# Kernel tuning notes

Hardware: AMD Instinct MI355X
Metric: run time of the kernel (lower is better)

## Reference

```python
import jax, jax.numpy as jnp
import numpy as np

N_HEAD = 16
HEAD_DIM = 64  # n_embd // n_head = 1024 // 16


def setup_inputs() -> dict:
    key = jax.random.key(0)
    k1, k2, k3 = jax.random.split(key, 3)
    B, T, C = 4, 2048, 1024
    x = jax.random.normal(k1, (B, T, C), dtype=jnp.float32)
    # torch Linear weight is (out, in); we store transposed (in, out) for x @ W
    w_qkv = jax.random.normal(k2, (C, 3 * C), dtype=jnp.float32) * (1.0 / np.sqrt(C))
    w_out = jax.random.normal(k3, (C, C), dtype=jnp.float32) * (1.0 / np.sqrt(C))
    return {"x": x, "w_qkv": w_qkv, "w_out": w_out}


def reference(x, w_qkv, w_out):
    B, T, C = x.shape
    scale = 1.0 / np.sqrt(HEAD_DIM).astype(np.float32)
    qkv = x @ w_qkv                                   # [B, T, 3C]
    q, k, v = jnp.split(qkv, 3, axis=2)
    def heads(t):  # [B, T, C] -> [B, H, T, Dh]
        return t.reshape(B, T, N_HEAD, HEAD_DIM).transpose(0, 2, 1, 3)
    q, k, v = heads(q), heads(k), heads(v)
    att = jnp.einsum('bhqd,bhkd->bhqk', q, k) * scale  # [B, H, T, T]
    causal = jnp.tril(jnp.ones((T, T), dtype=bool))
    att = jnp.where(causal[None, None], att, jnp.float32(-jnp.inf))
    att = jax.nn.softmax(att, axis=-1)
    y = jnp.einsum('bhqk,bhkd->bhqd', att, v)          # [B, H, T, Dh]
    y = y.transpose(0, 2, 1, 3).reshape(B, T, C)
    return y @ w_out
```

## Files before the change

### kernel.cpp

```cpp
#include <hip/hip_runtime.h>
#include <hip/hip_bf16.h>

#define B_ 4
#define T_ 2048
#define C_ 1024
#define H_ 16
#define D_ 64

typedef __bf16 bf16x8 __attribute__((ext_vector_type(8)));
typedef float f32x4 __attribute__((ext_vector_type(4)));

__device__ __forceinline__ unsigned short f2bs(float f) {
    __hip_bfloat16 h = __float2bfloat16(f);
    return *reinterpret_cast<unsigned short*>(&h);
}

__device__ __forceinline__ int swz(int row, int col) {
    return (row * 64 + col) ^ ((row & 7) << 3);
}

__device__ __forceinline__ void gload16(const void* g, void* l) {
    auto gp = (const __attribute__((address_space(1))) void*)(g);
    auto lp = (__attribute__((address_space(3))) void*)(uintptr_t)(l);
    __builtin_amdgcn_global_load_lds(gp, lp, 16, 0, 0);
}

__global__ __launch_bounds__(256)
void cvt_f32_to_bf16(const float* __restrict__ in, unsigned short* __restrict__ out, int n4) {
    int i = blockIdx.x * 256 + threadIdx.x;
    if (i >= n4) return;
    float4 v = ((const float4*)in)[i];
    union { unsigned short h[4]; uint2 u; } pk;
    pk.h[0] = f2bs(v.x); pk.h[1] = f2bs(v.y);
    pk.h[2] = f2bs(v.z); pk.h[3] = f2bs(v.w);
    ((uint2*)out)[i] = pk.u;
}

__global__ __launch_bounds__(256)
void transpose_to_bf16(const float* __restrict__ in, unsigned short* __restrict__ out,
                       int R, int C) {
    __shared__ float tile[64][65];
    const int tx = threadIdx.x & 63;
    const int ty = threadIdx.x >> 6;
    const int r0 = blockIdx.y * 64, c0 = blockIdx.x * 64;
    #pragma unroll
    for (int i = 0; i < 16; ++i) {
        int r = ty * 16 + i;
        tile[r][tx] = in[(size_t)(r0 + r) * C + c0 + tx];
    }
    __syncthreads();
    #pragma unroll
    for (int i = 0; i < 16; ++i) {
        int r = ty * 16 + i;
        out[(size_t)(c0 + r) * R + r0 + tx] = f2bs(tile[tx][r]);
    }
}

template<int MODE>
__global__ __launch_bounds__(256)
void gemm_bt(const unsigned short* __restrict__ A,
             const unsigned short* __restrict__ Bt,
             float* __restrict__ Out, int N_out,
             unsigned short* __restrict__ Qb,
             unsigned short* __restrict__ Kb,
             unsigned short* __restrict__ Vt,
             int K) {
    __shared__ alignas(16) unsigned short As[128 * 64];
    __shared__ alignas(16) unsigned short Bs[128 * 64];
    const int tid = threadIdx.x;
    const int l = tid & 63;
    const int c16 = l & 15, lq = l >> 4;
    const int wv = tid >> 6;
    const int wrow = wv >> 1, wcol = wv & 1;
    const int m0 = blockIdx.x * 128, n0 = blockIdx.y * 128;

    f32x4 acc[4][4];
    #pragma unroll
    for (int i = 0; i < 4; ++i)
        #pragma unroll
        for (int j = 0; j < 4; ++j)
            acc[i][j] = f32x4{0.f, 0.f, 0.f, 0.f};

    const int srow = tid >> 3;
    const int scs  = tid & 7;
    const int ldsbase = (tid & ~63) * 8;

    for (int k0 = 0; k0 < K; k0 += 64) {
        __syncthreads();
        #pragma unroll
        for (int p = 0; p < 4; ++p) {
            int row = p * 32 + srow;
            int csw = 8 * (scs ^ (row & 7));
            gload16(&A[(size_t)(m0 + row) * K + k0 + csw], &As[p * 2048 + ldsbase]);
            gload16(&Bt[(size_t)(n0 + row) * K + k0 + csw], &Bs[p * 2048 + ldsbase]);
        }
        __syncthreads();
        #pragma unroll
        for (int kk = 0; kk < 64; kk += 32) {
            bf16x8 af[4], bfv[4];
            int koff = kk + lq * 8;
            #pragma unroll
            for (int i = 0; i < 4; ++i) {
                af[i]  = *(const bf16x8*)&As[swz(wrow * 64 + i * 16 + c16, koff)];
                bfv[i] = *(const bf16x8*)&Bs[swz(wcol * 64 + i * 16 + c16, koff)];
            }
            #pragma unroll
            for (int mi = 0; mi < 4; ++mi)
                #pragma unroll
                for (int ni = 0; ni < 4; ++ni)
                    acc[mi][ni] = __builtin_amdgcn_mfma_f32_16x16x32_bf16(
                        af[mi], bfv[ni], acc[mi][ni], 0, 0, 0);
        }
    }

    #pragma unroll
    for (int mi = 0; mi < 4; ++mi) {
        #pragma unroll
        for (int ni = 0; ni < 4; ++ni) {
            #pragma unroll
            for (int r = 0; r < 4; ++r) {
                float v = acc[mi][ni][r];
                int row = m0 + wrow * 64 + mi * 16 + lq * 4 + r;
                int col = n0 + wcol * 64 + ni * 16 + c16;
                if (MODE == 1) {
                    Out[(size_t)row * N_out + col] = v;
                } else {
                    int which = col >> 10;
                    int c = col & 1023;
                    int h = c >> 6, d = c & 63;
                    int b = row >> 11, t = row & 2047;
                    int bh = b * H_ + h;
                    if (which == 0)
                        Qb[((size_t)(bh * T_ + t)) * D_ + d] = f2bs(v * 0.1803368801111204f);
                    else if (which == 1)
                        Kb[((size_t)(bh * T_ + t)) * D_ + d] = f2bs(v);
                    else
                        Vt[((size_t)(bh * D_ + d)) * T_ + t] = f2bs(v);
                }
            }
        }
    }
}

__global__ __launch_bounds__(256, 4)
void attn_fwd(const unsigned short* __restrict__ Qb,
              const unsigned short* __restrict__ Kb,
              const unsigned short* __restrict__ Vt,
              unsigned short* __restrict__ Y) {
    __shared__ alignas(16) unsigned short Ks[2][64 * 64];
    __shared__ alignas(16) unsigned short Vs[2][64 * 64];
    __shared__ alignas(16) unsigned short Pl[4][16 * 64];
    const int tid = threadIdx.x;
    const int wv = tid >> 6;
    const int l = tid & 63;
    const int c16 = l & 15, lq = l >> 4;
    const int bh = blockIdx.x & 63;
    const int qp = blockIdx.x >> 6;
    const unsigned short* Kp = Kb + (size_t)bh * T_ * D_;
    const unsigned short* Vp = Vt + (size_t)bh * D_ * T_;
    const unsigned short* Qbase = Qb + (size_t)bh * T_ * D_;
    const int b = bh >> 4, h = bh & 15;
    const int srow = tid >> 3;
    const int scs  = tid & 7;
    const int scol_sw = 8 * (scs ^ (srow & 7));
    const int wbase = wv * 512;
    unsigned short* Pw = (unsigned short*)Pl[wv];

    #pragma unroll
    for (int half = 0; half < 2; ++half) {
        const int qc = (half == 0) ? qp : 31 - qp;
        const int q0w = qc * 64 + wv * 16;
        const int nt = qc + 1;

        bf16x8 qf[2];
        #pragma unroll
        for (int ks = 0; ks < 2; ++ks)
            qf[ks] = *(const bf16x8*)&Qbase[(size_t)(q0w + c16) * 64 + 32 * ks + 8 * lq];

        f32x4 o[4];
        #pragma unroll
        for (int d0 = 0; d0 < 4; ++d0) o[d0] = f32x4{0.f, 0.f, 0.f, 0.f};
        float lsum = 0.f;

        __syncthreads();
        gload16(&Kp[(size_t)srow * 64 + scol_sw],        &Ks[0][wbase]);
        gload16(&Kp[(size_t)(srow + 32) * 64 + scol_sw], &Ks[0][2048 + wbase]);
        gload16(&Vp[(size_t)srow * T_ + scol_sw],        &Vs[0][wbase]);
        gload16(&Vp[(size_t)(srow + 32) * T_ + scol_sw], &Vs[0][2048 + wbase]);

        for (int it = 0; it < nt; ++it) {
            const int kb = it * 64;
            __syncthreads();
            if (it + 1 < nt) {
                const int kn = kb + 64;
                unsigned short* Kd = Ks[(it + 1) & 1];
                unsigned short* Vd = Vs[(it + 1) & 1];
                gload16(&Kp[(size_t)(kn + srow) * 64 + scol_sw],        &Kd[wbase]);
                gload16(&Kp[(size_t)(kn + srow + 32) * 64 + scol_sw],   &Kd[2048 + wbase]);
                gload16(&Vp[(size_t)srow * T_ + kn + scol_sw],          &Vd[wbase]);
                gload16(&Vp[(size_t)(srow + 32) * T_ + kn + scol_sw],   &Vd[2048 + wbase]);
            }
            const unsigned short* Kl = Ks[it & 1];
            const unsigned short* Vl = Vs[it & 1];

            f32x4 s[4];
            #pragma unroll
            for (int hh = 0; hh < 4; ++hh) s[hh] = f32x4{0.f, 0.f, 0.f, 0.f};
            __builtin_amdgcn_s_setprio(1);
            #pragma unroll
            for (int ks = 0; ks < 2; ++ks) {
                bf16x8 af[4];
                #pragma unroll
                for (int hh = 0; hh < 4; ++hh)
                    af[hh] = *(const bf16x8*)&Kl[swz(16 * hh + c16, 32 * ks + 8 * lq)];
                #pragma unroll
                for (int hh = 0; hh < 4; ++hh)
                    s[hh] = __builtin_amdgcn_mfma_f32_16x16x32_bf16(af[hh], qf[ks], s[hh], 0, 0, 0);
            }
            __builtin_amdgcn_s_setprio(0);
            if (it == nt - 1) {
                const int q = q0w + c16;
                #pragma unroll
                for (int hh = 0; hh < 4; ++hh)
                    #pragma unroll
                    for (int r = 0; r < 4; ++r)
                        if (kb + 16 * hh + 4 * lq + r > q) s[hh][r] = -1e30f;
            }
            float rs = 0.f;
            #pragma unroll
            for (int hh = 0; hh < 4; ++hh)
                #pragma unroll
                for (int r = 0; r < 4; ++r) {
                    float p = exp2f(s[hh][r]);
                    s[hh][r] = p;
                    rs += p;
                }
            lsum += rs;
            #pragma unroll
            for (int hh = 0; hh < 4; ++hh) {
                uint2 pk;
                pk.x = (unsigned)f2bs(s[hh][0]) | ((unsigned)f2bs(s[hh][1]) << 16);
                pk.y = (unsigned)f2bs(s[hh][2]) | ((unsigned)f2bs(s[hh][3]) << 16);
                *(uint2*)&Pw[swz(c16, 16 * hh + 4 * lq)] = pk;
            }
            __builtin_amdgcn_s_setprio(1);
            #pragma unroll
            for (int ks = 0; ks < 2; ++ks) {
                bf16x8 pb = *(const bf16x8*)&Pw[swz(c16, 32 * ks + 8 * lq)];
                #pragma unroll
                for (int d0 = 0; d0 < 4; ++d0) {
                    bf16x8 va = *(const bf16x8*)&Vl[swz(16 * d0 + c16, 32 * ks + 8 * lq)];
                    o[d0] = __builtin_amdgcn_mfma_f32_16x16x32_bf16(va, pb, o[d0], 0, 0, 0);
                }
            }
            __builtin_amdgcn_s_setprio(0);
        }

        float lt = lsum;
        lt += __shfl_xor(lt, 16);
        lt += __shfl_xor(lt, 32);
        float inv = 1.f / lt;
        int t = q0w + c16;
        #pragma unroll
        for (int d0 = 0; d0 < 4; ++d0) {
            uint2 w;
            w.x = (unsigned)f2bs(o[d0][0] * inv) | ((unsigned)f2bs(o[d0][1] * inv) << 16);
            w.y = (unsigned)f2bs(o[d0][2] * inv) | ((unsigned)f2bs(o[d0][3] * inv) << 16);
            *(uint2*)&Y[((size_t)(b * T_ + t)) * C_ + h * D_ + 16 * d0 + 4 * lq] = w;
        }
    }
}

extern "C" void kernel_launch(void* const* d_in, const int* in_sizes, int n_in,
                              void* d_out, int out_size, void* d_ws, size_t ws_size,
                              hipStream_t stream) {
    const float* x     = (const float*)d_in[0];
    const float* w_qkv = (const float*)d_in[1];
    const float* w_out = (const float*)d_in[2];
    float* out = (float*)d_out;
    char* ws = (char*)d_ws;

    unsigned short* xb  = (unsigned short*)(ws);
    unsigned short* wqt = (unsigned short*)(ws + (16u << 20));
    unsigned short* wot = (unsigned short*)(ws + (22u << 20));
    unsigned short* Qb  = (unsigned short*)(ws + (24u << 20));
    unsigned short* Kb  = (unsigned short*)(ws + (40u << 20));
    unsigned short* Vt  = (unsigned short*)(ws + (56u << 20));
    unsigned short* Yb  = (unsigned short*)(ws + (72u << 20));

    cvt_f32_to_bf16<<<8192, 256, 0, stream>>>(x, xb, (B_ * T_ * C_) / 4);
    transpose_to_bf16<<<dim3(48, 16), 256, 0, stream>>>(w_qkv, wqt, 1024, 3072);
    transpose_to_bf16<<<dim3(16, 16), 256, 0, stream>>>(w_out, wot, 1024, 1024);
    gemm_bt<0><<<dim3(64, 24), 256, 0, stream>>>(xb, wqt, nullptr, 3072, Qb, Kb, Vt, 1024);
    attn_fwd<<<1024, 256, 0, stream>>>(Qb, Kb, Vt, Yb);
    gemm_bt<1><<<dim3(64, 8), 256, 0, stream>>>(Yb, wot, out, 1024, nullptr, nullptr, nullptr, 1024);
}
```

Measured before the change: 186.5 us.

## Double-buffer GEMM LDS tiles and enlarge attention query tile to 128 rows

The GEMM now uses two LDS buffers so the next K-slice's global-to-LDS loads are issued before the current slice's MFMAs, which halves the barriers per iteration and overlaps load latency with compute. The attention kernel now has each wave handle 32 query rows (128 per block), reusing every loaded K/V tile for twice as many MFMAs. The grid is halved accordingly and waves skip fully masked key tiles. In exchange, register and LDS use per block grow, launch bounds drop to 2 blocks per SM, and fewer blocks may reduce latency hiding.

```diff
diff --git a/kernel.cpp b/kernel.cpp
--- a/kernel.cpp
+++ b/kernel.cpp
@@ -65,8 +65,8 @@
              unsigned short* __restrict__ Kb,
              unsigned short* __restrict__ Vt,
              int K) {
-    __shared__ alignas(16) unsigned short As[128 * 64];
-    __shared__ alignas(16) unsigned short Bs[128 * 64];
+    __shared__ alignas(16) unsigned short As[2][128 * 64];
+    __shared__ alignas(16) unsigned short Bs[2][128 * 64];
     const int tid = threadIdx.x;
     const int l = tid & 63;
     const int c16 = l & 15, lq = l >> 4;
@@ -85,24 +85,31 @@
     const int scs  = tid & 7;
     const int ldsbase = (tid & ~63) * 8;
 
-    for (int k0 = 0; k0 < K; k0 += 64) {
-        __syncthreads();
+    auto stage = [&](int k0, int buf) {
         #pragma unroll
         for (int p = 0; p < 4; ++p) {
             int row = p * 32 + srow;
             int csw = 8 * (scs ^ (row & 7));
-            gload16(&A[(size_t)(m0 + row) * K + k0 + csw], &As[p * 2048 + ldsbase]);
-            gload16(&Bt[(size_t)(n0 + row) * K + k0 + csw], &Bs[p * 2048 + ldsbase]);
-        }
+            gload16(&A[(size_t)(m0 + row) * K + k0 + csw], &As[buf][p * 2048 + ldsbase]);
+            gload16(&Bt[(size_t)(n0 + row) * K + k0 + csw], &Bs[buf][p * 2048 + ldsbase]);
+        }
+    };
+
+    stage(0, 0);
+    const int NK = K >> 6;
+    for (int i = 0; i < NK; ++i) {
         __syncthreads();
+        if (i + 1 < NK) stage((i + 1) << 6, (i + 1) & 1);
+        const unsigned short* Al = As[i & 1];
+        const unsigned short* Bl = Bs[i & 1];
         #pragma unroll
         for (int kk = 0; kk < 64; kk += 32) {
             bf16x8 af[4], bfv[4];
             int koff = kk + lq * 8;
             #pragma unroll
-            for (int i = 0; i < 4; ++i) {
-                af[i]  = *(const bf16x8*)&As[swz(wrow * 64 + i * 16 + c16, koff)];
-                bfv[i] = *(const bf16x8*)&Bs[swz(wcol * 64 + i * 16 + c16, koff)];
+            for (int t = 0; t < 4; ++t) {
+                af[t]  = *(const bf16x8*)&Al[swz(wrow * 64 + t * 16 + c16, koff)];
+                bfv[t] = *(const bf16x8*)&Bl[swz(wcol * 64 + t * 16 + c16, koff)];
             }
             #pragma unroll
             for (int mi = 0; mi < 4; ++mi)
@@ -142,14 +149,14 @@
     }
 }
 
-__global__ __launch_bounds__(256, 4)
+__global__ __launch_bounds__(256, 2)
 void attn_fwd(const unsigned short* __restrict__ Qb,
               const unsigned short* __restrict__ Kb,
               const unsigned short* __restrict__ Vt,
               unsigned short* __restrict__ Y) {
     __shared__ alignas(16) unsigned short Ks[2][64 * 64];
     __shared__ alignas(16) unsigned short Vs[2][64 * 64];
-    __shared__ alignas(16) unsigned short Pl[4][16 * 64];
+    __shared__ alignas(16) unsigned short Pl[4][32 * 64];
     const int tid = threadIdx.x;
     const int wv = tid >> 6;
     const int l = tid & 63;
@@ -168,19 +175,24 @@
 
     #pragma unroll
     for (int half = 0; half < 2; ++half) {
-        const int qc = (half == 0) ? qp : 31 - qp;
-        const int q0w = qc * 64 + wv * 16;
-        const int nt = qc + 1;
-
-        bf16x8 qf[2];
-        #pragma unroll
-        for (int ks = 0; ks < 2; ++ks)
-            qf[ks] = *(const bf16x8*)&Qbase[(size_t)(q0w + c16) * 64 + 32 * ks + 8 * lq];
-
-        f32x4 o[4];
-        #pragma unroll
-        for (int d0 = 0; d0 < 4; ++d0) o[d0] = f32x4{0.f, 0.f, 0.f, 0.f};
-        float lsum = 0.f;
+        const int qc = (half == 0) ? qp : 15 - qp;
+        const int q0w = qc * 128 + wv * 32;
+        const int nt = 2 * qc + 2;
+
+        bf16x8 qf[2][2];
+        #pragma unroll
+        for (int j = 0; j < 2; ++j)
+            #pragma unroll
+            for (int ks = 0; ks < 2; ++ks)
+                qf[j][ks] = *(const bf16x8*)&Qbase[(size_t)(q0w + 16 * j + c16) * 64 + 32 * ks + 8 * lq];
+
+        f32x4 o[4][2];
+        #pragma unroll
+        for (int d0 = 0; d0 < 4; ++d0)
+            #pragma unroll
+            for (int j = 0; j < 2; ++j)
+                o[d0][j] = f32x4{0.f, 0.f, 0.f, 0.f};
+        float lsum[2] = {0.f, 0.f};
 
         __syncthreads();
         gload16(&Kp[(size_t)srow * 64 + scol_sw],        &Ks[0][wbase]);
@@ -200,12 +212,16 @@
                 gload16(&Vp[(size_t)srow * T_ + kn + scol_sw],          &Vd[wbase]);
                 gload16(&Vp[(size_t)(srow + 32) * T_ + kn + scol_sw],   &Vd[2048 + wbase]);
             }
+            if (kb > q0w + 31) continue;
             const unsigned short* Kl = Ks[it & 1];
             const unsigned short* Vl = Vs[it & 1];
 
-            f32x4 s[4];
-            #pragma unroll
-            for (int hh = 0; hh < 4; ++hh) s[hh] = f32x4{0.f, 0.f, 0.f, 0.f};
+            f32x4 s[4][2];
+            #pragma unroll
+            for (int hh = 0; hh < 4; ++hh)
+                #pragma unroll
+                for (int j = 0; j < 2; ++j)
+                    s[hh][j] = f32x4{0.f, 0.f, 0.f, 0.f};
             __builtin_amdgcn_s_setprio(1);
             #pragma unroll
             for (int ks = 0; ks < 2; ++ks) {
@@ -215,58 +231,78 @@
                     af[hh] = *(const bf16x8*)&Kl[swz(16 * hh + c16, 32 * ks + 8 * lq)];
                 #pragma unroll
                 for (int hh = 0; hh < 4; ++hh)
-                    s[hh] = __builtin_amdgcn_mfma_f32_16x16x32_bf16(af[hh], qf[ks], s[hh], 0, 0, 0);
+                    #pragma unroll
+                    for (int j = 0; j < 2; ++j)
+                        s[hh][j] = __builtin_amdgcn_mfma_f32_16x16x32_bf16(
+                            af[hh], qf[j][ks], s[hh][j], 0, 0, 0);
             }
             __builtin_amdgcn_s_setprio(0);
-            if (it == nt - 1) {
-                const int q = q0w + c16;
+            if (kb + 63 > q0w) {
                 #pragma unroll
                 for (int hh = 0; hh < 4; ++hh)
                     #pragma unroll
-                    for (int r = 0; r < 4; ++r)
-                        if (kb + 16 * hh + 4 * lq + r > q) s[hh][r] = -1e30f;
-            }
-            float rs = 0.f;
+                    for (int j = 0; j < 2; ++j) {
+                        const int q = q0w + 16 * j + c16;
+                        #pragma unroll
+                        for (int r = 0; r < 4; ++r)
+                            if (kb + 16 * hh + 4 * lq + r > q) s[hh][j][r] = -1e30f;
+                    }
+            }
+            #pragma unroll
+            for (int j = 0; j < 2; ++j) {
+                float rs = 0.f;
+                #pragma unroll
+                for (int hh = 0; hh < 4; ++hh)
+                    #pragma unroll
+                    for (int r = 0; r < 4; ++r) {
+                        float p = exp2f(s[hh][j][r]);
+                        s[hh][j][r] = p;
+                        rs += p;
+                    }
+                lsum[j] += rs;
+            }
             #pragma unroll
             for (int hh = 0; hh < 4; ++hh)
                 #pragma unroll
-                for (int r = 0; r < 4; ++r) {
-                    float p = exp2f(s[hh][r]);
-                    s[hh][r] = p;
-                    rs += p;
+                for (int j = 0; j < 2; ++j) {
+                    uint2 pk;
+                    pk.x = (unsigned)f2bs(s[hh][j][0]) | ((unsigned)f2bs(s[hh][j][1]) << 16);
+                    pk.y = (unsigned)f2bs(s[hh][j][2]) | ((unsigned)f2bs(s[hh][j][3]) << 16);
+                    *(uint2*)&Pw[swz(16 * j + c16, 16 * hh + 4 * lq)] = pk;
                 }
-            lsum += rs;
-            #pragma unroll
-            for (int hh = 0; hh < 4; ++hh) {
-                uint2 pk;
-                pk.x = (unsigned)f2bs(s[hh][0]) | ((unsigned)f2bs(s[hh][1]) << 16);
-                pk.y = (unsigned)f2bs(s[hh][2]) | ((unsigned)f2bs(s[hh][3]) << 16);
-                *(uint2*)&Pw[swz(c16, 16 * hh + 4 * lq)] = pk;
-            }
             __builtin_amdgcn_s_setprio(1);
             #pragma unroll
             for (int ks = 0; ks < 2; ++ks) {
-                bf16x8 pb = *(const bf16x8*)&Pw[swz(c16, 32 * ks + 8 * lq)];
+                bf16x8 pb[2];
+                #pragma unroll
+                for (int j = 0; j < 2; ++j)
+                    pb[j] = *(const bf16x8*)&Pw[swz(16 * j + c16, 32 * ks + 8 * lq)];
                 #pragma unroll
                 for (int d0 = 0; d0 < 4; ++d0) {
                     bf16x8 va = *(const bf16x8*)&Vl[swz(16 * d0 + c16, 32 * ks + 8 * lq)];
-                    o[d0] = __builtin_amdgcn_mfma_f32_16x16x32_bf16(va, pb, o[d0], 0, 0, 0);
+                    #pragma unroll
+                    for (int j = 0; j < 2; ++j)
+                        o[d0][j] = __builtin_amdgcn_mfma_f32_16x16x32_bf16(
+                            va, pb[j], o[d0][j], 0, 0, 0);
                 }
             }
             __builtin_amdgcn_s_setprio(0);
         }
 
-        float lt = lsum;
-        lt += __shfl_xor(lt, 16);
-        lt += __shfl_xor(lt, 32);
-        float inv = 1.f / lt;
-        int t = q0w + c16;
-        #pragma unroll
-        for (int d0 = 0; d0 < 4; ++d0) {
-            uint2 w;
-            w.x = (unsigned)f2bs(o[d0][0] * inv) | ((unsigned)f2bs(o[d0][1] * inv) << 16);
-            w.y = (unsigned)f2bs(o[d0][2] * inv) | ((unsigned)f2bs(o[d0][3] * inv) << 16);
-            *(uint2*)&Y[((size_t)(b * T_ + t)) * C_ + h * D_ + 16 * d0 + 4 * lq] = w;
+        #pragma unroll
+        for (int j = 0; j < 2; ++j) {
+            float lt = lsum[j];
+            lt += __shfl_xor(lt, 16);
+            lt += __shfl_xor(lt, 32);
+            float inv = 1.f / lt;
+            int t = q0w + 16 * j + c16;
+            #pragma unroll
+            for (int d0 = 0; d0 < 4; ++d0) {
+                uint2 w;
+                w.x = (unsigned)f2bs(o[d0][j][0] * inv) | ((unsigned)f2bs(o[d0][j][1] * inv) << 16);
+                w.y = (unsigned)f2bs(o[d0][j][2] * inv) | ((unsigned)f2bs(o[d0][j][3] * inv) << 16);
+                *(uint2*)&Y[((size_t)(b * T_ + t)) * C_ + h * D_ + 16 * d0 + 4 * lq] = w;
+            }
         }
     }
 }
@@ -292,6 +328,6 @@
     transpose_to_bf16<<<dim3(48, 16), 256, 0, stream>>>(w_qkv, wqt, 1024, 3072);
     transpose_to_bf16<<<dim3(16, 16), 256, 0, stream>>>(w_out, wot, 1024, 1024);
     gemm_bt<0><<<dim3(64, 24), 256, 0, stream>>>(xb, wqt, nullptr, 3072, Qb, Kb, Vt, 1024);
-    attn_fwd<<<1024, 256, 0, stream>>>(Qb, Kb, Vt, Yb);
+    attn_fwd<<<512, 256, 0, stream>>>(Qb, Kb, Vt, Yb);
     gemm_bt<1><<<dim3(64, 8), 256, 0, stream>>>(Yb, wot, out, 1024, nullptr, nullptr, nullptr, 1024);
 }
```

Result: faster. 178.7 us (-4.2%).

## Double-buffer GEMM LDS tiles and merge weight transpose launches

Applied to the files above, without the earlier changes.

The bf16 GEMM now keeps two LDS buffers for the A and B tiles. It issues the asynchronous global-to-LDS loads for the next K tile before running the MFMAs on the current one, so load latency overlaps compute and one barrier per iteration is removed. The two weight transpose kernels are merged into a single launch that picks its source by block index, saving one launch. The cost is doubled LDS use per block (64KB), which may reduce the number of resident blocks per CU.

```diff
diff --git a/kernel.cpp b/kernel.cpp
--- a/kernel.cpp
+++ b/kernel.cpp
@@ -37,12 +37,18 @@
 }
 
 __global__ __launch_bounds__(256)
-void transpose_to_bf16(const float* __restrict__ in, unsigned short* __restrict__ out,
-                       int R, int C) {
+void transpose_weights(const float* __restrict__ in1, unsigned short* __restrict__ out1,
+                       const float* __restrict__ in2, unsigned short* __restrict__ out2) {
     __shared__ float tile[64][65];
     const int tx = threadIdx.x & 63;
     const int ty = threadIdx.x >> 6;
-    const int r0 = blockIdx.y * 64, c0 = blockIdx.x * 64;
+    const bool second = blockIdx.x >= 48;
+    const float* in = second ? in2 : in1;
+    unsigned short* out = second ? out2 : out1;
+    const int C = second ? 1024 : 3072;
+    const int R = 1024;
+    const int c0 = (second ? (blockIdx.x - 48) : blockIdx.x) * 64;
+    const int r0 = blockIdx.y * 64;
     #pragma unroll
     for (int i = 0; i < 16; ++i) {
         int r = ty * 16 + i;
@@ -65,8 +71,8 @@
              unsigned short* __restrict__ Kb,
              unsigned short* __restrict__ Vt,
              int K) {
-    __shared__ alignas(16) unsigned short As[128 * 64];
-    __shared__ alignas(16) unsigned short Bs[128 * 64];
+    __shared__ alignas(16) unsigned short As[2][128 * 64];
+    __shared__ alignas(16) unsigned short Bs[2][128 * 64];
     const int tid = threadIdx.x;
     const int l = tid & 63;
     const int c16 = l & 15, lq = l >> 4;
@@ -85,24 +91,31 @@
     const int scs  = tid & 7;
     const int ldsbase = (tid & ~63) * 8;
 
-    for (int k0 = 0; k0 < K; k0 += 64) {
-        __syncthreads();
+    auto stage = [&](int k0, int buf) {
         #pragma unroll
         for (int p = 0; p < 4; ++p) {
             int row = p * 32 + srow;
             int csw = 8 * (scs ^ (row & 7));
-            gload16(&A[(size_t)(m0 + row) * K + k0 + csw], &As[p * 2048 + ldsbase]);
-            gload16(&Bt[(size_t)(n0 + row) * K + k0 + csw], &Bs[p * 2048 + ldsbase]);
-        }
+            gload16(&A[(size_t)(m0 + row) * K + k0 + csw], &As[buf][p * 2048 + ldsbase]);
+            gload16(&Bt[(size_t)(n0 + row) * K + k0 + csw], &Bs[buf][p * 2048 + ldsbase]);
+        }
+    };
+
+    stage(0, 0);
+    const int NK = K >> 6;
+    for (int i = 0; i < NK; ++i) {
         __syncthreads();
+        if (i + 1 < NK) stage((i + 1) << 6, (i + 1) & 1);
+        const unsigned short* Al = As[i & 1];
+        const unsigned short* Bl = Bs[i & 1];
         #pragma unroll
         for (int kk = 0; kk < 64; kk += 32) {
             bf16x8 af[4], bfv[4];
             int koff = kk + lq * 8;
             #pragma unroll
-            for (int i = 0; i < 4; ++i) {
-                af[i]  = *(const bf16x8*)&As[swz(wrow * 64 + i * 16 + c16, koff)];
-                bfv[i] = *(const bf16x8*)&Bs[swz(wcol * 64 + i * 16 + c16, koff)];
+            for (int t = 0; t < 4; ++t) {
+                af[t]  = *(const bf16x8*)&Al[swz(wrow * 64 + t * 16 + c16, koff)];
+                bfv[t] = *(const bf16x8*)&Bl[swz(wcol * 64 + t * 16 + c16, koff)];
             }
             #pragma unroll
             for (int mi = 0; mi < 4; ++mi)
@@ -289,8 +302,7 @@
     unsigned short* Yb  = (unsigned short*)(ws + (72u << 20));
 
     cvt_f32_to_bf16<<<8192, 256, 0, stream>>>(x, xb, (B_ * T_ * C_) / 4);
-    transpose_to_bf16<<<dim3(48, 16), 256, 0, stream>>>(w_qkv, wqt, 1024, 3072);
-    transpose_to_bf16<<<dim3(16, 16), 256, 0, stream>>>(w_out, wot, 1024, 1024);
+    transpose_weights<<<dim3(64, 16), 256, 0, stream>>>(w_qkv, wqt, w_out, wot);
     gemm_bt<0><<<dim3(64, 24), 256, 0, stream>>>(xb, wqt, nullptr, 3072, Qb, Kb, Vt, 1024);
     attn_fwd<<<1024, 256, 0, stream>>>(Qb, Kb, Vt, Yb);
     gemm_bt<1><<<dim3(64, 8), 256, 0, stream>>>(Yb, wot, out, 1024, nullptr, nullptr, nullptr, 1024);
```

Measured after the change: 179.3 us. 3.8% less time.
